# Performance work log

Hardware: AMD Instinct MI355X
Metric: run time of the kernel (lower is better)

Reference implementation:

```python
import jax, jax.numpy as jnp
import numpy as np

HEADS = 8
HEAD_DIM = 64
WINDOW = 65  # odd


def setup_inputs() -> dict:
    key = jax.random.key(0)
    k1, k2, k3 = jax.random.split(key, 3)
    B, S, D_MODEL = 2, 2048, HEADS * HEAD_DIM
    x = jax.random.normal(k1, (B, S, D_MODEL), dtype=jnp.float32)
    W_qkv = jax.random.normal(k2, (D_MODEL, 3 * HEADS * HEAD_DIM), dtype=jnp.float32) * (1.0 / np.sqrt(D_MODEL))
    W_out = jax.random.normal(k3, (HEADS * HEAD_DIM, D_MODEL), dtype=jnp.float32) * (1.0 / np.sqrt(HEADS * HEAD_DIM))
    b_out = jnp.zeros((D_MODEL,), dtype=jnp.float32)
    return {"x": x, "W_qkv": W_qkv, "W_out": W_out, "b_out": b_out}


def reference(x, W_qkv, W_out, b_out):
    B, S, _ = x.shape
    H, D, W = HEADS, HEAD_DIM, WINDOW
    pad = W // 2

    qkv = x @ W_qkv                              # [B,S,3*H*D]
    qkv = qkv.reshape(B, S, H, 3 * D)
    q, k, v = jnp.split(qkv, 3, axis=-1)          # each [B,S,H,D]

    # zero-pad along sequence (matches tf.pad; padded keys get score 0, NOT -inf)
    k_pad = jnp.pad(k, ((0, 0), (pad, pad), (0, 0), (0, 0)))
    v_pad = jnp.pad(v, ((0, 0), (pad, pad), (0, 0), (0, 0)))

    # sliding windows via gather: [S, W] indices into padded seq (= tf.signal.frame)
    idx = jnp.arange(S)[:, None] + jnp.arange(W)[None, :]
    k_win = k_pad[:, idx]                         # [B,S,W,H,D]
    v_win = v_pad[:, idx]                         # [B,S,W,H,D]

    scale = 1.0 / jnp.sqrt(jnp.asarray(D, dtype=x.dtype))
    scores = jnp.einsum('bshd,bswhd->bhsw', q, k_win) * scale  # [B,H,S,W]
    weights = jax.nn.softmax(scores, axis=-1)
    attn = jnp.einsum('bhsw,bswhd->bshd', weights, v_win)       # [B,S,H,D]
    attn = attn.reshape(B, S, H * D)
    return attn @ W_out + b_out
```

## Files before the change

kernel.cpp:

```cpp
#include <hip/hip_runtime.h>
#include <hip/hip_bf16.h>
#include <stdint.h>

typedef short short8 __attribute__((ext_vector_type(8)));
typedef float f32x4 __attribute__((ext_vector_type(4)));
typedef unsigned short ushort4_t __attribute__((ext_vector_type(4)));
typedef unsigned short ushort8_t __attribute__((ext_vector_type(8)));

#define S_LEN 2048
#define NQKV 1536
#define DMODEL 512

__device__ inline unsigned short f2bf(float f) {
  unsigned int u = __float_as_uint(f);
  unsigned int r = (u + 0x7FFFu + ((u >> 16) & 1u)) >> 16;
  return (unsigned short)r;
}

__device__ __forceinline__ void gll16(const unsigned short* g, unsigned short* l) {
  __builtin_amdgcn_global_load_lds(
      (const __attribute__((address_space(1))) unsigned int*)g,
      (__attribute__((address_space(3))) unsigned int*)l, 16, 0, 0);
}

__global__ __launch_bounds__(256) void k_prep(const float* __restrict__ x,
                                              unsigned short* __restrict__ xb,
                                              const float* __restrict__ w1,
                                              unsigned short* __restrict__ o1,
                                              const float* __restrict__ w2,
                                              unsigned short* __restrict__ o2,
                                              unsigned short* __restrict__ Kp,
                                              unsigned short* __restrict__ Vp) {
  __shared__ float T[32][33];
  int bid = blockIdx.x;
  int t = threadIdx.x;
  if (bid < 1024) {
    int i = (bid * 256 + t) * 8;
    float4 a = *(const float4*)(x + i);
    float4 b = *(const float4*)(x + i + 4);
    ushort8_t o;
    o[0] = f2bf(a.x); o[1] = f2bf(a.y); o[2] = f2bf(a.z); o[3] = f2bf(a.w);
    o[4] = f2bf(b.x); o[5] = f2bf(b.y); o[6] = f2bf(b.z); o[7] = f2bf(b.w);
    *(ushort8_t*)(xb + i) = o;
    return;
  }
  if (bid >= 2048) {
    int p = bid - 2048;
    ushort8_t z = {};
    if (p < 16) {
      unsigned short* dst = Kp + (size_t)p * 2112 * 64;
#pragma unroll
      for (int i = 0; i < 2; i++) {
        int s = t + 256 * i;
        int row = s >> 3, c = s & 7;
        int r2 = row < 32 ? row : row - 32 + 2080;
        *(ushort8_t*)&dst[r2 * 64 + c * 8] = z;
      }
    } else {
      unsigned short* dst = Vp + (size_t)(p - 16) * 64 * 2112;
#pragma unroll
      for (int i = 0; i < 2; i++) {
        int s = t + 256 * i;
        int d = s >> 3, side = (s >> 2) & 1, c = s & 3;
        *(ushort8_t*)&dst[(size_t)d * 2112 + side * 2080 + c * 8] = z;
      }
    }
    return;
  }
  bid -= 1024;
  int bx = bid & 63, byy = bid >> 6;
  const float* w; unsigned short* o; int cols;
  if (bx < 48) { w = w1; o = o1; cols = 1536; }
  else         { w = w2; o = o2; cols = 512; bx -= 48; }
  int r0 = byy * 32, c0 = bx * 32;
  int tr = t / 32, tc = t % 32;
#pragma unroll
  for (int i = 0; i < 4; i++) {
    int r = tr + i * 8;
    T[r][tc] = w[(size_t)(r0 + r) * cols + c0 + tc];
  }
  __syncthreads();
#pragma unroll
  for (int i = 0; i < 4; i++) {
    int rr = tr + i * 8;
    o[(size_t)(c0 + rr) * 512 + r0 + tc] = f2bf(T[tc][rr]);
  }
}

template <int BM, int BN, int MODE>
__global__ __launch_bounds__(256) void k_gemm(const unsigned short* __restrict__ A,
                                              const unsigned short* __restrict__ Bt,
                                              void* __restrict__ Cout,
                                              const float* __restrict__ bias,
                                              unsigned short* __restrict__ qs,
                                              unsigned short* __restrict__ kp,
                                              unsigned short* __restrict__ vp,
                                              int M, int N, int K) {
  constexpr int MR = BM / 32, NR = BN / 32;
  constexpr int CA = BM / 32, CB = BN / 32;
  constexpr int STAGE_SH = 2 * (BM + BN) * 64;
  constexpr int BOUNCE_SH = MODE == 0 ? BM * BN * 2 : BM * BN;
  constexpr int SMEM_SH = STAGE_SH > BOUNCE_SH ? STAGE_SH : BOUNCE_SH;
  __shared__ __align__(16) unsigned short smem[SMEM_SH];
  const int ASZ = BM * 64, BOFF = 2 * BM * 64, BSZ = BN * 64;

  const int t = threadIdx.x, lane = t & 63, wid = t >> 6;
  const int m0 = blockIdx.y * BM, n0 = blockIdx.x * BN;
  const int wm = (wid >> 1) * (BM / 2), wn = (wid & 1) * (BN / 2);
  const int lr = lane & 15, lg = lane >> 4;
  const unsigned short* Ab = A + (size_t)m0 * K;
  const unsigned short* Bb = Bt + (size_t)n0 * K;
  f32x4 acc[MR][NR] = {};

  const int NT = K / 64;
  auto stage = [&](int buf, int kt) {
#pragma unroll
    for (int c = 0; c < CA; c++) {
      int f = t + 256 * c;
      int row = f >> 3, ch = f & 7;
      gll16(Ab + (size_t)row * K + kt + ((ch ^ (row & 7)) << 3),
            &smem[buf * ASZ + f * 8]);
    }
#pragma unroll
    for (int c = 0; c < CB; c++) {
      int f = t + 256 * c;
      int row = f >> 3, ch = f & 7;
      gll16(Bb + (size_t)row * K + kt + ((ch ^ (row & 7)) << 3),
            &smem[BOFF + buf * BSZ + f * 8]);
    }
  };

  stage(0, 0);
  int buf = 0;
  for (int it = 0; it < NT; ++it) {
    __syncthreads();
    if (it + 1 < NT) stage(buf ^ 1, (it + 1) * 64);
    const unsigned short* Ap = &smem[buf * ASZ];
    const unsigned short* Bp = &smem[BOFF + buf * BSZ];
#pragma unroll
    for (int sl = 0; sl < 2; sl++) {
      const int cs = sl * 4 + lg;
      short8 af[MR], bfv[NR];
#pragma unroll
      for (int i = 0; i < MR; i++) {
        int row = wm + i * 16 + lr;
        af[i] = *(const short8*)&Ap[row * 64 + ((cs ^ (row & 7)) << 3)];
      }
#pragma unroll
      for (int i = 0; i < NR; i++) {
        int row = wn + i * 16 + lr;
        bfv[i] = *(const short8*)&Bp[row * 64 + ((cs ^ (row & 7)) << 3)];
      }
#pragma unroll
      for (int mi = 0; mi < MR; mi++)
#pragma unroll
        for (int ni = 0; ni < NR; ni++)
          acc[mi][ni] = __builtin_amdgcn_mfma_f32_16x16x32_bf16(af[mi], bfv[ni], acc[mi][ni], 0, 0, 0);
    }
    buf ^= 1;
  }

  if (MODE == 0) {
    __syncthreads();
    float* ft = (float*)smem;
#pragma unroll
    for (int mi = 0; mi < MR; mi++)
#pragma unroll
      for (int ni = 0; ni < NR; ni++)
#pragma unroll
        for (int j = 0; j < 4; j++)
          ft[(wm + mi * 16 + lg * 4 + j) * BN + wn + ni * 16 + lr] = acc[mi][ni][j];
    __syncthreads();
#pragma unroll
    for (int i = 0; i < BM * BN / 1024; i++) {
      int s = t + 256 * i;
      int row = s / (BN / 4), ch = s % (BN / 4);
      float4 v = *(const float4*)&ft[row * BN + ch * 4];
      float4 bv = *(const float4*)&bias[n0 + ch * 4];
      v.x += bv.x; v.y += bv.y; v.z += bv.z; v.w += bv.w;
      *(float4*)&((float*)Cout)[(size_t)(m0 + row) * N + n0 + ch * 4] = v;
    }
  } else {
    __syncthreads();
#pragma unroll
    for (int mi = 0; mi < MR; mi++)
#pragma unroll
      for (int ni = 0; ni < NR; ni++)
#pragma unroll
        for (int j = 0; j < 4; j++) {
          int row = wm + mi * 16 + lg * 4 + j;
          int col = wn + ni * 16 + lr;
          smem[row * 64 + (((col >> 3) ^ ((row >> 3) & 7)) << 3) + (col & 7)] =
              f2bf(acc[mi][ni][j]);
        }
    __syncthreads();

    const int b_ = m0 >> 11;
    const int posb = m0 & 2047;
    const int h = n0 / 192, seg = (n0 % 192) >> 6;
    if (seg < 2) {
      unsigned short* dst = (seg == 0)
          ? qs + ((size_t)(b_ * 8 + h) * 2048 + posb) * 64
          : kp + ((size_t)(b_ * 8 + h) * 2112 + 32 + posb) * 64;
#pragma unroll
      for (int i = 0; i < BM / 32; i++) {
        int s = t + 256 * i;
        int row = s >> 3, ch = s & 7;
        int src = row * 64 + ((ch ^ ((row >> 3) & 7)) << 3);
        *(ushort8_t*)&dst[s * 8] = *(const ushort8_t*)&smem[src];
      }
    } else {
      unsigned short* dst = vp + (size_t)(b_ * 8 + h) * 64 * 2112;
#pragma unroll
      for (int i = 0; i < BM / 32; i++) {
        int s = t + 256 * i;
        int dl = s / (BM / 8), pc = s % (BM / 8);
        ushort8_t v;
#pragma unroll
        for (int j = 0; j < 8; j++) {
          int row = pc * 8 + j;
          v[j] = smem[row * 64 + ((((dl >> 3) ^ (pc & 7)) << 3)) + (dl & 7)];
        }
        *(ushort8_t*)&dst[(size_t)dl * 2112 + 32 + posb + pc * 8] = v;
      }
    }
  }
}

__global__ __launch_bounds__(512) void k_attn(const unsigned short* __restrict__ Qs,
                                              const unsigned short* __restrict__ Kp,
                                              const unsigned short* __restrict__ Vp,
                                              unsigned short* __restrict__ attnb) {
  __shared__ __align__(16) unsigned short Kt[192 * 64];
  __shared__ __align__(16) unsigned short Vt[64 * 256];
  __shared__ __align__(16) unsigned short Qt[128 * 64];
  const int t = threadIdx.x, lane = t & 63, w = t >> 6;
  const int blk = blockIdx.x;
  const int sbi = blk & 15, h = (blk >> 4) & 7, b = blk >> 7;
  const int sb = sbi * 128;
  const int bh = b * 8 + h;
  const int lr = lane & 15, lg = lane >> 4;

  {
    const unsigned short* src = Kp + ((size_t)bh * 2112 + sb) * 64;
#pragma unroll
    for (int i = 0; i < 3; i++) {
      int s = t + 512 * i, row = s >> 3, c = s & 7;
      gll16(src + row * 64 + (c ^ (row & 7)) * 8, &Kt[s * 8]);
    }
  }
  {
    const unsigned short* src = Vp + (size_t)bh * 64 * 2112 + sb;
#pragma unroll
    for (int i = 0; i < 4; i++) {
      int s = t + 512 * i, d = s >> 5, c = s & 31;
      gll16(src + (size_t)d * 2112 + (c ^ (d & 7)) * 8, &Vt[s * 8]);
    }
  }
  {
    const unsigned short* src = Qs + ((size_t)bh * 2048 + sb) * 64;
#pragma unroll
    for (int i = 0; i < 2; i++) {
      int s = t + 512 * i, row = s >> 3, c = s & 7;
      gll16(src + row * 64 + (c ^ (row & 7)) * 8, &Qt[s * 8]);
    }
  }
  __syncthreads();

  const int sw = (lr & 7) << 3;

  short8 qb[2];
#pragma unroll
  for (int ks = 0; ks < 2; ks++)
    qb[ks] = *(const short8*)&Qt[(w * 16 + lr) * 64 + ((ks * 32 + lg * 8) ^ sw)];

  f32x4 sc[5] = {};
#pragma unroll
  for (int ct = 0; ct < 5; ct++) {
#pragma unroll
    for (int ks = 0; ks < 2; ks++) {
      short8 ka = *(const short8*)&Kt[(w * 16 + ct * 16 + lr) * 64 + ((ks * 32 + lg * 8) ^ sw)];
      sc[ct] = __builtin_amdgcn_mfma_f32_16x16x32_bf16(ka, qb[ks], sc[ct], 0, 0, 0);
    }
  }

  float mx = -1e30f;
#pragma unroll
  for (int ct = 0; ct < 5; ct++)
#pragma unroll
    for (int j = 0; j < 4; j++) {
      int c2 = ct * 16 + lg * 4 + j;
      sc[ct][j] = (c2 >= lr && c2 <= lr + 64) ? sc[ct][j] * 0.125f : -1e30f;
      mx = fmaxf(mx, sc[ct][j]);
    }
  mx = fmaxf(mx, __shfl_xor(mx, 16, 64));
  mx = fmaxf(mx, __shfl_xor(mx, 32, 64));

  float pn[5][4];
  float sum = 0.0f;
#pragma unroll
  for (int ct = 0; ct < 5; ct++)
#pragma unroll
    for (int j = 0; j < 4; j++) {
      pn[ct][j] = __expf(sc[ct][j] - mx);
      sum += pn[ct][j];
    }
  sum += __shfl_xor(sum, 16, 64);
  sum += __shfl_xor(sum, 32, 64);
  float inv = 1.0f / sum;

  unsigned int w01[5], w23[5];
#pragma unroll
  for (int ct = 0; ct < 5; ct++) {
    w01[ct] = (unsigned int)f2bf(pn[ct][0] * inv) | ((unsigned int)f2bf(pn[ct][1] * inv) << 16);
    w23[ct] = (unsigned int)f2bf(pn[ct][2] * inv) | ((unsigned int)f2bf(pn[ct][3] * inv) << 16);
  }

  f32x4 oa[4] = {};
  const int h2 = lg & 1, tl = lg >> 1;
  const int sA = 32 * h2 + lr, sB = sA + 16;
#pragma unroll
  for (int ks = 0; ks < 3; ks++) {
    const int T0 = 2 * ks;
    const int T1 = (2 * ks + 1 < 5) ? (2 * ks + 1) : 4;
    unsigned int a0 = __shfl((int)w01[T0], sA, 64), a1 = __shfl((int)w23[T0], sA, 64);
    unsigned int a2 = __shfl((int)w01[T0], sB, 64), a3 = __shfl((int)w23[T0], sB, 64);
    unsigned int b0 = __shfl((int)w01[T1], sA, 64), b1 = __shfl((int)w23[T1], sA, 64);
    unsigned int b2 = __shfl((int)w01[T1], sB, 64), b3 = __shfl((int)w23[T1], sB, 64);
    union { unsigned int u[4]; short8 v; } pb;
    pb.u[0] = tl ? b0 : a0;
    pb.u[1] = tl ? b1 : a1;
    pb.u[2] = tl ? b2 : a2;
    pb.u[3] = tl ? b3 : a3;
    if (ks == 2 && tl) { pb.u[0] = 0; pb.u[1] = 0; pb.u[2] = 0; pb.u[3] = 0; }
    int pofl = w * 16 + ks * 32 + lg * 8;
#pragma unroll
    for (int nt = 0; nt < 4; nt++) {
      short8 va = *(const short8*)&Vt[(nt * 16 + lr) * 256 + (pofl ^ sw)];
      oa[nt] = __builtin_amdgcn_mfma_f32_16x16x32_bf16(va, pb.v, oa[nt], 0, 0, 0);
    }
  }

  const int s0 = sb + w * 16;
#pragma unroll
  for (int nt = 0; nt < 4; nt++) {
    ushort4_t o;
#pragma unroll
    for (int j = 0; j < 4; j++) o[j] = f2bf(oa[nt][j]);
    *(ushort4_t*)&attnb[((size_t)b * S_LEN + s0 + lr) * DMODEL + h * 64 + nt * 16 + lg * 4] = o;
  }
}

extern "C" void kernel_launch(void* const* d_in, const int* in_sizes, int n_in,
                              void* d_out, int out_size, void* d_ws, size_t ws_size,
                              hipStream_t stream) {
  const float* x    = (const float*)d_in[0];
  const float* Wqkv = (const float*)d_in[1];
  const float* Wout = (const float*)d_in[2];
  const float* bout = (const float*)d_in[3];
  char* ws = (char*)d_ws;
  unsigned short* xb    = (unsigned short*)(ws + 0);
  unsigned short* wqkvt = (unsigned short*)(ws + 4194304);
  unsigned short* woutt = (unsigned short*)(ws + 5767168);
  unsigned short* Qs    = (unsigned short*)(ws + 6291456);
  unsigned short* Kp    = (unsigned short*)(ws + 10485760);
  unsigned short* Vp    = (unsigned short*)(ws + 14811136);
  unsigned short* attnb = (unsigned short*)(ws + 19922944);

  hipLaunchKernelGGL(k_prep, dim3(2080), dim3(256), 0, stream,
                     x, xb, Wqkv, wqkvt, Wout, woutt, Kp, Vp);
  hipLaunchKernelGGL((k_gemm<128, 64, 1>), dim3(24, 32), dim3(256), 0, stream,
                     xb, wqkvt, nullptr, (const float*)nullptr, Qs, Kp, Vp, 4096, 1536, 512);
  hipLaunchKernelGGL(k_attn, dim3(256), dim3(512), 0, stream, Qs, Kp, Vp, attnb);
  hipLaunchKernelGGL((k_gemm<64, 64, 0>), dim3(8, 64), dim3(256), 0, stream,
                     attnb, woutt, d_out, bout,
                     (unsigned short*)nullptr, (unsigned short*)nullptr,
                     (unsigned short*)nullptr, 4096, 512, 512);
}
```

Baseline: 36.58 us.

## Load GEMM B operand and attention Q directly from global into registers

The GEMM kernel stops staging the B tile through LDS. Each wave now loads its B fragments straight from global memory into registers, double-buffered across a loop unrolled by two, which also shrinks LDS use and adds an occupancy hint of 3 blocks per CU. The attention kernel likewise drops the Q LDS tile and reads Q fragments directly into registers. This removes LDS traffic and footprint, at the cost of uncoalesced global loads duplicated across waves and more register pressure. The unrolled-by-two loop also assumes an even tile count along K.

```diff
diff --git a/kernel.cpp b/kernel.cpp
--- a/kernel.cpp
+++ b/kernel.cpp
@@ -88,21 +88,21 @@
 }
 
 template <int BM, int BN, int MODE>
-__global__ __launch_bounds__(256) void k_gemm(const unsigned short* __restrict__ A,
-                                              const unsigned short* __restrict__ Bt,
-                                              void* __restrict__ Cout,
-                                              const float* __restrict__ bias,
-                                              unsigned short* __restrict__ qs,
-                                              unsigned short* __restrict__ kp,
-                                              unsigned short* __restrict__ vp,
-                                              int M, int N, int K) {
+__global__ __launch_bounds__(256, 3) void k_gemm(const unsigned short* __restrict__ A,
+                                                 const unsigned short* __restrict__ Bt,
+                                                 void* __restrict__ Cout,
+                                                 const float* __restrict__ bias,
+                                                 unsigned short* __restrict__ qs,
+                                                 unsigned short* __restrict__ kp,
+                                                 unsigned short* __restrict__ vp,
+                                                 int M, int N, int K) {
   constexpr int MR = BM / 32, NR = BN / 32;
-  constexpr int CA = BM / 32, CB = BN / 32;
-  constexpr int STAGE_SH = 2 * (BM + BN) * 64;
+  constexpr int CA = BM / 32;
+  constexpr int STAGE_SH = 2 * BM * 64;
   constexpr int BOUNCE_SH = MODE == 0 ? BM * BN * 2 : BM * BN;
   constexpr int SMEM_SH = STAGE_SH > BOUNCE_SH ? STAGE_SH : BOUNCE_SH;
   __shared__ __align__(16) unsigned short smem[SMEM_SH];
-  const int ASZ = BM * 64, BOFF = 2 * BM * 64, BSZ = BN * 64;
+  const int ASZ = BM * 64;
 
   const int t = threadIdx.x, lane = t & 63, wid = t >> 6;
   const int m0 = blockIdx.y * BM, n0 = blockIdx.x * BN;
@@ -121,43 +121,45 @@
       gll16(Ab + (size_t)row * K + kt + ((ch ^ (row & 7)) << 3),
             &smem[buf * ASZ + f * 8]);
     }
-#pragma unroll
-    for (int c = 0; c < CB; c++) {
-      int f = t + 256 * c;
-      int row = f >> 3, ch = f & 7;
-      gll16(Bb + (size_t)row * K + kt + ((ch ^ (row & 7)) << 3),
-            &smem[BOFF + buf * BSZ + f * 8]);
-    }
   };
-
-  stage(0, 0);
-  int buf = 0;
-  for (int it = 0; it < NT; ++it) {
-    __syncthreads();
-    if (it + 1 < NT) stage(buf ^ 1, (it + 1) * 64);
+  auto loadB = [&](int kt, short8 (&bv)[2][NR]) {
+#pragma unroll
+    for (int sl = 0; sl < 2; sl++)
+#pragma unroll
+      for (int i = 0; i < NR; i++) {
+        int row = wn + i * 16 + lr;
+        bv[sl][i] = *(const short8*)(Bb + (size_t)row * K + kt + (sl * 4 + lg) * 8);
+      }
+  };
+  auto compute = [&](int buf, short8 (&bv)[2][NR]) {
     const unsigned short* Ap = &smem[buf * ASZ];
-    const unsigned short* Bp = &smem[BOFF + buf * BSZ];
 #pragma unroll
     for (int sl = 0; sl < 2; sl++) {
       const int cs = sl * 4 + lg;
-      short8 af[MR], bfv[NR];
+      short8 af[MR];
 #pragma unroll
       for (int i = 0; i < MR; i++) {
         int row = wm + i * 16 + lr;
         af[i] = *(const short8*)&Ap[row * 64 + ((cs ^ (row & 7)) << 3)];
       }
 #pragma unroll
-      for (int i = 0; i < NR; i++) {
-        int row = wn + i * 16 + lr;
-        bfv[i] = *(const short8*)&Bp[row * 64 + ((cs ^ (row & 7)) << 3)];
-      }
-#pragma unroll
       for (int mi = 0; mi < MR; mi++)
 #pragma unroll
         for (int ni = 0; ni < NR; ni++)
-          acc[mi][ni] = __builtin_amdgcn_mfma_f32_16x16x32_bf16(af[mi], bfv[ni], acc[mi][ni], 0, 0, 0);
-    }
-    buf ^= 1;
+          acc[mi][ni] = __builtin_amdgcn_mfma_f32_16x16x32_bf16(af[mi], bv[sl][ni], acc[mi][ni], 0, 0, 0);
+    }
+  };
+
+  short8 b0[2][NR], b1[2][NR];
+  stage(0, 0);
+  loadB(0, b0);
+  for (int it = 0; it < NT; it += 2) {
+    __syncthreads();
+    if (it + 1 < NT) { stage(1, (it + 1) * 64); loadB((it + 1) * 64, b1); }
+    compute(0, b0);
+    __syncthreads();
+    if (it + 2 < NT) { stage(0, (it + 2) * 64); loadB((it + 2) * 64, b0); }
+    compute(1, b1);
   }
 
   if (MODE == 0) {
@@ -233,7 +235,6 @@
                                               unsigned short* __restrict__ attnb) {
   __shared__ __align__(16) unsigned short Kt[192 * 64];
   __shared__ __align__(16) unsigned short Vt[64 * 256];
-  __shared__ __align__(16) unsigned short Qt[128 * 64];
   const int t = threadIdx.x, lane = t & 63, w = t >> 6;
   const int blk = blockIdx.x;
   const int sbi = blk & 15, h = (blk >> 4) & 7, b = blk >> 7;
@@ -241,6 +242,11 @@
   const int bh = b * 8 + h;
   const int lr = lane & 15, lg = lane >> 4;
 
+  short8 qb[2];
+#pragma unroll
+  for (int ks = 0; ks < 2; ks++)
+    qb[ks] = *(const short8*)(Qs + ((size_t)bh * 2048 + sb + w * 16 + lr) * 64 + ks * 32 + lg * 8);
+
   {
     const unsigned short* src = Kp + ((size_t)bh * 2112 + sb) * 64;
 #pragma unroll
@@ -257,22 +263,9 @@
       gll16(src + (size_t)d * 2112 + (c ^ (d & 7)) * 8, &Vt[s * 8]);
     }
   }
-  {
-    const unsigned short* src = Qs + ((size_t)bh * 2048 + sb) * 64;
-#pragma unroll
-    for (int i = 0; i < 2; i++) {
-      int s = t + 512 * i, row = s >> 3, c = s & 7;
-      gll16(src + row * 64 + (c ^ (row & 7)) * 8, &Qt[s * 8]);
-    }
-  }
   __syncthreads();
 
   const int sw = (lr & 7) << 3;
-
-  short8 qb[2];
-#pragma unroll
-  for (int ks = 0; ks < 2; ks++)
-    qb[ks] = *(const short8*)&Qt[(w * 16 + lr) * 64 + ((ks * 32 + lg * 8) ^ sw)];
 
   f32x4 sc[5] = {};
 #pragma unroll
```

Result: slower. 47.15 us (+28.9%).
